# Kernel optimization log

Hardware: AMD Instinct MI355X
Metric: run time of the kernel (lower is better)

The kernel has to match this reference:

```python
import jax, jax.numpy as jnp
import numpy as np

B, N, C_IN, HID, K, DEG = 8192, 64, 128, 128, 5, 8


def setup_inputs() -> dict:
    key = jax.random.key(0)
    ks = jax.random.split(key, 8)
    total = B * N
    E = B * N * DEG
    x = jax.random.normal(ks[0], (total, C_IN), dtype=jnp.float32)
    batch = jnp.repeat(jnp.arange(B, dtype=jnp.int64), N)
    g = jnp.repeat(jnp.arange(B, dtype=jnp.int64), N * DEG)
    src = g * N + jax.random.randint(ks[1], (E,), 0, N).astype(jnp.int64)
    dst = g * N + jax.random.randint(ks[2], (E,), 0, N).astype(jnp.int64)
    edge_index = jnp.stack([src, dst])  # [2, E]
    s = 0.05
    return {
        "x": x,
        "edge_index": edge_index,
        "batch": batch,
        "W_pool": jax.random.normal(ks[3], (C_IN, K), dtype=jnp.float32) * s,
        "b_pool": jnp.zeros((K,), jnp.float32),
        "W1": jax.random.normal(ks[4], (C_IN, HID), dtype=jnp.float32) * s,
        "b1": jnp.zeros((HID,), jnp.float32),
        "W2": jax.random.normal(ks[5], (HID, HID), dtype=jnp.float32) * s,
        "b2": jnp.zeros((HID,), jnp.float32),
        "W_lin": jax.random.normal(ks[6], (HID, 1), dtype=jnp.float32) * s,
        "b_lin": jnp.zeros((1,), jnp.float32),
        "num_graphs": B,
        "max_nodes": N,
    }


def dense_gcn(x, adj, W, b, mask=None):
    # PyG DenseGCNConv with add_loop=True: diagonal set to 1 on a copy
    n = adj.shape[1]
    idx = jnp.arange(n)
    adj_l = adj.at[:, idx, idx].set(1.0)
    out = x @ W  # [B, n, out]
    d = jnp.clip(adj_l.sum(-1), 1.0) ** -0.5  # [B, n]
    adj_n = d[:, :, None] * adj_l * d[:, None, :]
    out = jnp.einsum('bnm,bmc->bnc', adj_n, out) + b
    if mask is not None:
        out = out * mask[..., None]
    return out


def reference(x, edge_index, batch, W_pool, b_pool, W1, b1, W2, b2, W_lin, b_lin,
              num_graphs, max_nodes):
    total = x.shape[0]
    # to_dense_batch: position of each node within its graph (batch is sorted)
    first_idx = jax.ops.segment_min(jnp.arange(total), batch, num_segments=num_graphs)
    pos = jnp.arange(total) - first_idx[batch]
    x_dense = jnp.zeros((num_graphs, max_nodes, x.shape[1]), x.dtype).at[batch, pos].set(x)
    mask = jnp.zeros((num_graphs, max_nodes), x.dtype).at[batch, pos].set(1.0)
    # to_dense_adj
    src, dst = edge_index[0], edge_index[1]
    adj = jnp.zeros((num_graphs, max_nodes, max_nodes), x.dtype)
    adj = adj.at[batch[src], pos[src], pos[dst]].add(1.0)

    s = dense_gcn(x_dense, adj, W_pool, b_pool, mask)       # [B, N, K]
    x_l1 = dense_gcn(x_dense, adj, W1, b1, mask)            # [B, N, H]

    # dense_diff_pool (losses are discarded by the original forward)
    s = jax.nn.softmax(s, axis=-1) * mask[..., None]
    xm = x_l1 * mask[..., None]
    x_p1 = jnp.einsum('bnk,bnc->bkc', s, xm)                # [B, K, H]
    adj_p1 = jnp.einsum('bnk,bnm,bml->bkl', s, adj, s)      # [B, K, K]

    x_l2 = dense_gcn(x_p1, adj_p1, W2, b2)                  # [B, K, H]
    pooled = x_l2.sum(axis=1)                               # global_add_pool -> [B, H]
    return pooled @ W_lin + b_lin                           # [B, 1]
```

## Files before the change

kernel.cpp:

```cpp
#include <hip/hip_runtime.h>
#include <hip/hip_bf16.h>

#define NN 64
#define CI 128
#define HD 128
#define KC 5
#define AJW 17

#define WS_Y   1024
#define WS_B1Z 1152
#define WS_B2W 1153

typedef float v4f __attribute__((ext_vector_type(4)));
typedef __bf16 v8bf __attribute__((ext_vector_type(8)));
typedef unsigned short us8 __attribute__((ext_vector_type(8)));

__device__ __forceinline__ unsigned short f2us(float f) {
    __hip_bfloat16 h = __float2bfloat16(f);
    return *reinterpret_cast<unsigned short*>(&h);
}

extern "C" __global__ void zprep(const float* __restrict__ W1,
                                 const float* __restrict__ Wp,
                                 const float* __restrict__ W2,
                                 const float* __restrict__ Wl,
                                 const float* __restrict__ b1,
                                 const float* __restrict__ b2,
                                 float* __restrict__ ws)
{
    const int t = threadIdx.x;
    __shared__ float sz_[HD];
    float a0 = 0.f, a1 = 0.f;
    for (int c = 0; c < HD; ++c) {
        const float wl = Wl[c];
        a0 += W2[t * HD + c] * wl;
        a1 += W2[(t + 64) * HD + c] * wl;
    }
    sz_[t] = a0; sz_[t + 64] = a1;
    float p1 = b1[t] * a0 + b1[t + 64] * a1;
    float p2 = b2[t] * Wl[t] + b2[t + 64] * Wl[t + 64];
    #pragma unroll
    for (int off = 32; off; off >>= 1) {
        p1 += __shfl_down(p1, off, 64);
        p2 += __shfl_down(p2, off, 64);
    }
    if (t == 0) { ws[WS_B1Z] = p1; ws[WS_B2W] = p2; }
    __syncthreads();
    #pragma unroll
    for (int rr = 0; rr < 2; ++rr) {
        const int r = t + rr * 64;
        float acc = 0.f;
        for (int h2 = 0; h2 < HD; ++h2) acc += W1[r * HD + h2] * sz_[h2];
        ws[WS_Y + r] = acc;
    }
    const int q = t >> 4, m16 = t & 15;
    #pragma unroll
    for (int ks = 0; ks < 4; ++ks) {
        const int k0 = ks * 32 + q * 8;
        us8 pk;
        #pragma unroll
        for (int j = 0; j < 8; ++j)
            pk[j] = f2us((m16 < KC) ? Wp[(k0 + j) * KC + m16] : 0.f);
        reinterpret_cast<us8*>(ws)[ks * 64 + t] = pk;
    }
}

extern "C" __global__ __launch_bounds__(256, 8)
void diffpool_main(const float* __restrict__ x,
                   const int* __restrict__ ei,
                   const float* __restrict__ bp,
                   const float* __restrict__ bl,
                   const float* __restrict__ ws,
                   float* __restrict__ out,
                   int E, int epg)
{
    __shared__ unsigned int sadjb[NN][AJW];
    __shared__ float sA [4][NN * KC];
    __shared__ float sBu[4][NN * KC];
    __shared__ float sc [4][NN];
    __shared__ float spp[4][25];
    __shared__ float sSm[NN][KC];
    __shared__ float sq[NN];
    __shared__ float sd[NN];
    __shared__ unsigned int srdeg[NN];
    __shared__ float sz_[HD];
    __shared__ float sadjp[25];
    __shared__ float sd2[KC];
    __shared__ float scoef[KC];

    const int t = threadIdx.x;
    const int g = blockIdx.x;
    const int lane = t & 63;
    const int wv = t >> 6;
    const int q4 = lane >> 4;
    const int m16 = lane & 15;
    const int n = lane;
    const int h = wv;
    const int arow = wv * 16 + m16;

    const float bp0 = bp[0], bp1 = bp[1], bp2 = bp[2], bp3 = bp[3], bp4 = bp[4];
    const float c_b1z = ws[WS_B1Z], c_b2w = ws[WS_B2W], c_bl = bl[0];

    int e0s = -1, e0d = 0, e1s = -1, e1d = 0;
    const int base = g * epg;
    if (t < epg)       { e0s = ei[base + t] & 63;        e0d = ei[E + base + t] & 63; }
    if (t + 256 < epg) { e1s = ei[base + t + 256] & 63;  e1d = ei[E + base + t + 256] & 63; }

    {
        unsigned int* ap = &sadjb[0][0];
        for (int i = t; i < NN * AJW; i += 256) ap[i] = 0u;
        if (t < NN) srdeg[t] = 0u;
        if (t < 32)
            reinterpret_cast<float4*>(sz_)[t] = reinterpret_cast<const float4*>(ws + WS_Y)[t];
    }
    __syncthreads();

    {
        if (e0s >= 0) {
            atomicAdd(&sadjb[e0s][e0d >> 2], 1u << ((e0d & 3) * 8));
            atomicAdd(&srdeg[e0s], 1u);
        }
        if (e1s >= 0) {
            atomicAdd(&sadjb[e1s][e1d >> 2], 1u << ((e1d & 3) * 8));
            atomicAdd(&srdeg[e1s], 1u);
        }
        for (int j = t + 512; j < epg; j += 256) {
            const int sn = ei[base + j] & 63;
            const int dn = ei[E + base + j] & 63;
            atomicAdd(&sadjb[sn][dn >> 2], 1u << ((dn & 3) * 8));
            atomicAdd(&srdeg[sn], 1u);
        }
    }
    {
        const float* xr = x + (size_t)g * (NN * CI) + arow * CI;
        const v8bf* wpk = reinterpret_cast<const v8bf*>(ws);
        v4f acc = {0.f, 0.f, 0.f, 0.f};
        float qp = 0.f;
        #pragma unroll
        for (int ks = 0; ks < 4; ++ks) {
            const int c0 = ks * 32 + q4 * 8;
            const float4 v0 = *reinterpret_cast<const float4*>(xr + c0);
            const float4 v1 = *reinterpret_cast<const float4*>(xr + c0 + 4);
            const float4 y0 = *reinterpret_cast<const float4*>(sz_ + c0);
            const float4 y1 = *reinterpret_cast<const float4*>(sz_ + c0 + 4);
            qp += v0.x * y0.x + v0.y * y0.y + v0.z * y0.z + v0.w * y0.w
                + v1.x * y1.x + v1.y * y1.y + v1.z * y1.z + v1.w * y1.w;
            us8 pk;
            pk[0] = f2us(v0.x); pk[1] = f2us(v0.y); pk[2] = f2us(v0.z); pk[3] = f2us(v0.w);
            pk[4] = f2us(v1.x); pk[5] = f2us(v1.y); pk[6] = f2us(v1.z); pk[7] = f2us(v1.w);
            const v8bf af = *reinterpret_cast<const v8bf*>(&pk);
            acc = __builtin_amdgcn_mfma_f32_16x16x32_bf16(af, wpk[ks * 64 + lane], acc, 0, 0, 0);
        }
        qp += __shfl_xor(qp, 16, 64);
        qp += __shfl_xor(qp, 32, 64);
        if (q4 == 0) sq[arow] = qp;
        if (m16 < KC) {
            #pragma unroll
            for (int r = 0; r < 4; ++r)
                sSm[wv * 16 + q4 * 4 + r][m16] = acc[r];
        }
    }
    __syncthreads();

    unsigned aw0, aw1, aw2, aw3;
    float dlane;
    {
        const unsigned selfb = (sadjb[lane][lane >> 2] >> ((lane & 3) * 8)) & 255u;
        dlane = rsqrtf((float)(srdeg[lane] + 1u - selfb));
        sd[lane] = dlane;
        aw0 = sadjb[n][h * 4 + 0];
        aw1 = sadjb[n][h * 4 + 1];
        aw2 = sadjb[n][h * 4 + 2];
        aw3 = sadjb[n][h * 4 + 3];
        float a0 = 0.f, a1 = 0.f, a2 = 0.f, a3 = 0.f, a4 = 0.f, cp = 0.f;
        #pragma unroll
        for (int i = 0; i < 4; ++i) {
            const unsigned w = (i == 0) ? aw0 : (i == 1) ? aw1 : (i == 2) ? aw2 : aw3;
            #pragma unroll
            for (int bb = 0; bb < 4; ++bb) {
                const int m = h * 16 + i * 4 + bb;
                const float al = (m == n) ? 1.f : (float)((w >> (bb * 8)) & 255u);
                const float f = al * sd[m];
                a0 += f * sSm[m][0]; a1 += f * sSm[m][1]; a2 += f * sSm[m][2];
                a3 += f * sSm[m][3]; a4 += f * sSm[m][4];
                cp += f * sq[m];
            }
        }
        float* pp = &sA[h][n * KC];
        pp[0] = a0; pp[1] = a1; pp[2] = a2; pp[3] = a3; pp[4] = a4;
        sc[h][n] = cp;
    }
    __syncthreads();

    float s0v, s1v, s2v, s3v, s4v;
    {
        float a0 = sA[0][n*KC+0] + sA[1][n*KC+0] + sA[2][n*KC+0] + sA[3][n*KC+0];
        float a1 = sA[0][n*KC+1] + sA[1][n*KC+1] + sA[2][n*KC+1] + sA[3][n*KC+1];
        float a2 = sA[0][n*KC+2] + sA[1][n*KC+2] + sA[2][n*KC+2] + sA[3][n*KC+2];
        float a3 = sA[0][n*KC+3] + sA[1][n*KC+3] + sA[2][n*KC+3] + sA[3][n*KC+3];
        float a4 = sA[0][n*KC+4] + sA[1][n*KC+4] + sA[2][n*KC+4] + sA[3][n*KC+4];
        a0 = a0 * dlane + bp0; a1 = a1 * dlane + bp1; a2 = a2 * dlane + bp2;
        a3 = a3 * dlane + bp3; a4 = a4 * dlane + bp4;
        const float mx = fmaxf(fmaxf(fmaxf(a0, a1), fmaxf(a2, a3)), a4);
        a0 = expf(a0 - mx); a1 = expf(a1 - mx); a2 = expf(a2 - mx);
        a3 = expf(a3 - mx); a4 = expf(a4 - mx);
        const float inv = 1.f / (a0 + a1 + a2 + a3 + a4);
        s0v = a0 * inv; s1v = a1 * inv; s2v = a2 * inv; s3v = a3 * inv; s4v = a4 * inv;
        sSm[n][0] = s0v; sSm[n][1] = s1v; sSm[n][2] = s2v;
        sSm[n][3] = s3v; sSm[n][4] = s4v;
        float u0 = 0.f, u1 = 0.f, u2 = 0.f, u3 = 0.f, u4 = 0.f;
        #pragma unroll
        for (int i = 0; i < 4; ++i) {
            const unsigned w = (i == 0) ? aw0 : (i == 1) ? aw1 : (i == 2) ? aw2 : aw3;
            #pragma unroll
            for (int bb = 0; bb < 4; ++bb) {
                const int m = h * 16 + i * 4 + bb;
                const float c = (float)((w >> (bb * 8)) & 255u);
                u0 += c * sSm[m][0]; u1 += c * sSm[m][1]; u2 += c * sSm[m][2];
                u3 += c * sSm[m][3]; u4 += c * sSm[m][4];
            }
        }
        float* pp = &sBu[h][n * KC];
        pp[0] = u0; pp[1] = u1; pp[2] = u2; pp[3] = u3; pp[4] = u4;
    }
    __syncthreads();

    if (lane < 25) {
        const int k = lane / 5, l = lane - k * 5;
        float a = 0.f;
        #pragma unroll
        for (int i = 0; i < 16; ++i) {
            const int m = h * 16 + i;
            const float uu = sBu[0][m*KC+l] + sBu[1][m*KC+l]
                           + sBu[2][m*KC+l] + sBu[3][m*KC+l];
            a += sSm[m][k] * uu;
        }
        spp[h][lane] = a;
    }
    __syncthreads();

    {
        if (lane < 25)
            sadjp[lane] = spp[0][lane] + spp[1][lane] + spp[2][lane] + spp[3][lane];
        if (lane < KC) {
            float s_ = 0.f;
            #pragma unroll
            for (int l = 0; l < KC; ++l) s_ += sadjp[lane * KC + l];
            s_ += 1.f - sadjp[lane * 6];
            sd2[lane] = rsqrtf(fmaxf(s_, 1.f));
        }
        if (lane < KC) {
            float a = 0.f;
            #pragma unroll
            for (int k = 0; k < KC; ++k) a += sd2[k] * sadjp[k * KC + lane];
            a += sd2[lane] * (1.f - sadjp[lane * 6]);
            scoef[lane] = sd2[lane] * a;
        }
        const float t5 = scoef[0] * s0v + scoef[1] * s1v + scoef[2] * s2v +
                         scoef[3] * s3v + scoef[4] * s4v;
        const float wn = dlane * t5;
        const float cfull = sc[0][n] + sc[1][n] + sc[2][n] + sc[3][n];
        float cb = t5;
        float v = wn * cfull;
        #pragma unroll
        for (int off = 32; off; off >>= 1) {
            cb += __shfl_down(cb, off, 64);
            v  += __shfl_down(v,  off, 64);
        }
        if (wv == 0 && lane == 0)
            out[g] = v + cb * c_b1z + 5.f * c_b2w + c_bl;
    }
}

extern "C" void kernel_launch(void* const* d_in, const int* in_sizes, int n_in,
                              void* d_out, int out_size, void* d_ws, size_t ws_size,
                              hipStream_t stream) {
    const float* x  = (const float*)d_in[0];
    const int*   ei = (const int*)d_in[1];
    const float* Wp = (const float*)d_in[3];
    const float* bp = (const float*)d_in[4];
    const float* W1 = (const float*)d_in[5];
    const float* b1 = (const float*)d_in[6];
    const float* W2 = (const float*)d_in[7];
    const float* b2 = (const float*)d_in[8];
    const float* Wl = (const float*)d_in[9];
    const float* bl = (const float*)d_in[10];
    float* out = (float*)d_out;
    float* ws  = (float*)d_ws;

    const int B = out_size;
    const int E = in_sizes[1] / 2;
    const int epg = E / B;

    zprep<<<1, 64, 0, stream>>>(W1, Wp, W2, Wl, b1, b2, ws);
    diffpool_main<<<B, 256, 0, stream>>>(x, ei, bp, bl, ws, out, E, epg);
}
```

Measured before the change: 453.4 us.

## Replace bf16 MFMA node projection with fp32 FMA and shuffle reduction

The per-graph projection of x onto the five pooling weights and the fused readout vector now uses fp32 FMAs. Each 16-lane group holds one 48-float slice of a combined 128x6 weight matrix, and partial sums are reduced with cross-lane shuffles. This replaces the bf16 MFMA path, removing the bf16 conversion of x and the shared-memory staging of the readout vector. It costs more VALU work, 24 shuffles per row group and many more registers, so the launch bound is lowered to 6 blocks per SM.

```diff
diff --git a/kernel.cpp b/kernel.cpp
--- a/kernel.cpp
+++ b/kernel.cpp
@@ -7,18 +7,9 @@
 #define KC 5
 #define AJW 17
 
-#define WS_Y   1024
-#define WS_B1Z 1152
-#define WS_B2W 1153
-
-typedef float v4f __attribute__((ext_vector_type(4)));
-typedef __bf16 v8bf __attribute__((ext_vector_type(8)));
-typedef unsigned short us8 __attribute__((ext_vector_type(8)));
-
-__device__ __forceinline__ unsigned short f2us(float f) {
-    __hip_bfloat16 h = __float2bfloat16(f);
-    return *reinterpret_cast<unsigned short*>(&h);
-}
+#define WS_WC  0
+#define WS_B1Z 768
+#define WS_B2W 769
 
 extern "C" __global__ void zprep(const float* __restrict__ W1,
                                  const float* __restrict__ Wp,
@@ -51,21 +42,13 @@
         const int r = t + rr * 64;
         float acc = 0.f;
         for (int h2 = 0; h2 < HD; ++h2) acc += W1[r * HD + h2] * sz_[h2];
-        ws[WS_Y + r] = acc;
-    }
-    const int q = t >> 4, m16 = t & 15;
-    #pragma unroll
-    for (int ks = 0; ks < 4; ++ks) {
-        const int k0 = ks * 32 + q * 8;
-        us8 pk;
-        #pragma unroll
-        for (int j = 0; j < 8; ++j)
-            pk[j] = f2us((m16 < KC) ? Wp[(k0 + j) * KC + m16] : 0.f);
-        reinterpret_cast<us8*>(ws)[ks * 64 + t] = pk;
+        #pragma unroll
+        for (int k = 0; k < KC; ++k) ws[WS_WC + r * 6 + k] = Wp[r * KC + k];
+        ws[WS_WC + r * 6 + 5] = acc;
     }
 }
 
-extern "C" __global__ __launch_bounds__(256, 8)
+extern "C" __global__ __launch_bounds__(256, 6)
 void diffpool_main(const float* __restrict__ x,
                    const int* __restrict__ ei,
                    const float* __restrict__ bp,
@@ -79,11 +62,10 @@
     __shared__ float sBu[4][NN * KC];
     __shared__ float sc [4][NN];
     __shared__ float spp[4][25];
-    __shared__ float sSm[NN][KC];
+    __shared__ float sSm[NN][6];
     __shared__ float sq[NN];
     __shared__ float sd[NN];
     __shared__ unsigned int srdeg[NN];
-    __shared__ float sz_[HD];
     __shared__ float sadjp[25];
     __shared__ float sd2[KC];
     __shared__ float scoef[KC];
@@ -92,11 +74,9 @@
     const int g = blockIdx.x;
     const int lane = t & 63;
     const int wv = t >> 6;
-    const int q4 = lane >> 4;
-    const int m16 = lane & 15;
+    const int ch = t & 15;
     const int n = lane;
     const int h = wv;
-    const int arow = wv * 16 + m16;
 
     const float bp0 = bp[0], bp1 = bp[1], bp2 = bp[2], bp3 = bp[3], bp4 = bp[4];
     const float c_b1z = ws[WS_B1Z], c_b2w = ws[WS_B2W], c_bl = bl[0];
@@ -110,8 +90,6 @@
         unsigned int* ap = &sadjb[0][0];
         for (int i = t; i < NN * AJW; i += 256) ap[i] = 0u;
         if (t < NN) srdeg[t] = 0u;
-        if (t < 32)
-            reinterpret_cast<float4*>(sz_)[t] = reinterpret_cast<const float4*>(ws + WS_Y)[t];
     }
     __syncthreads();
 
@@ -130,34 +108,44 @@
             atomicAdd(&sadjb[sn][dn >> 2], 1u << ((dn & 3) * 8));
             atomicAdd(&srdeg[sn], 1u);
         }
-    }
-    {
-        const float* xr = x + (size_t)g * (NN * CI) + arow * CI;
-        const v8bf* wpk = reinterpret_cast<const v8bf*>(ws);
-        v4f acc = {0.f, 0.f, 0.f, 0.f};
-        float qp = 0.f;
-        #pragma unroll
-        for (int ks = 0; ks < 4; ++ks) {
-            const int c0 = ks * 32 + q4 * 8;
-            const float4 v0 = *reinterpret_cast<const float4*>(xr + c0);
-            const float4 v1 = *reinterpret_cast<const float4*>(xr + c0 + 4);
-            const float4 y0 = *reinterpret_cast<const float4*>(sz_ + c0);
-            const float4 y1 = *reinterpret_cast<const float4*>(sz_ + c0 + 4);
-            qp += v0.x * y0.x + v0.y * y0.y + v0.z * y0.z + v0.w * y0.w
-                + v1.x * y1.x + v1.y * y1.y + v1.z * y1.z + v1.w * y1.w;
-            us8 pk;
-            pk[0] = f2us(v0.x); pk[1] = f2us(v0.y); pk[2] = f2us(v0.z); pk[3] = f2us(v0.w);
-            pk[4] = f2us(v1.x); pk[5] = f2us(v1.y); pk[6] = f2us(v1.z); pk[7] = f2us(v1.w);
-            const v8bf af = *reinterpret_cast<const v8bf*>(&pk);
-            acc = __builtin_amdgcn_mfma_f32_16x16x32_bf16(af, wpk[ks * 64 + lane], acc, 0, 0, 0);
-        }
-        qp += __shfl_xor(qp, 16, 64);
-        qp += __shfl_xor(qp, 32, 64);
-        if (q4 == 0) sq[arow] = qp;
-        if (m16 < KC) {
-            #pragma unroll
-            for (int r = 0; r < 4; ++r)
-                sSm[wv * 16 + q4 * 4 + r][m16] = acc[r];
+        float wc[48];
+        {
+            const float4* wc4 = reinterpret_cast<const float4*>(ws + WS_WC + ch * 48);
+            #pragma unroll
+            for (int i4 = 0; i4 < 12; ++i4)
+                *reinterpret_cast<float4*>(&wc[i4 * 4]) = wc4[i4];
+        }
+        const float* xg = x + (size_t)g * (NN * CI);
+        #pragma unroll
+        for (int i = 0; i < 4; ++i) {
+            const int row = (t >> 4) + 16 * i;
+            const float* xr = xg + row * CI + ch * 8;
+            const float4 v0 = *reinterpret_cast<const float4*>(xr);
+            const float4 v1 = *reinterpret_cast<const float4*>(xr + 4);
+            float acc[6];
+            #pragma unroll
+            for (int k = 0; k < 6; ++k) acc[k] = 0.f;
+            #pragma unroll
+            for (int k = 0; k < 6; ++k) {
+                acc[k] += v0.x * wc[0 * 6 + k] + v0.y * wc[1 * 6 + k]
+                        + v0.z * wc[2 * 6 + k] + v0.w * wc[3 * 6 + k]
+                        + v1.x * wc[4 * 6 + k] + v1.y * wc[5 * 6 + k]
+                        + v1.z * wc[6 * 6 + k] + v1.w * wc[7 * 6 + k];
+            }
+            #pragma unroll
+            for (int k = 0; k < 6; ++k) {
+                float r = acc[k];
+                r += __shfl_xor(r, 1, 16);
+                r += __shfl_xor(r, 2, 16);
+                r += __shfl_xor(r, 4, 16);
+                r += __shfl_xor(r, 8, 16);
+                acc[k] = r;
+            }
+            float val = acc[0];
+            #pragma unroll
+            for (int k = 1; k < 6; ++k) val = (ch == k) ? acc[k] : val;
+            if (ch < KC)       sSm[row][ch] = val;
+            else if (ch == 5)  sq[row] = val;
         }
     }
     __syncthreads();
```

Measured after the change: 425.6 us. -6.1%, faster.
